# Kernel tuning notes

Hardware: AMD Instinct MI355X
Metric: run time of the kernel (lower is better)

## Reference

```python
import jax, jax.numpy as jnp
import numpy as np

HIDDEN = 128
N_RBF = 32
LMAX = 2
N_NODES = 10000
DEG = 8  # each node has DEG outgoing (and DEG incoming) edges on a ring


def _build_graph():
    src = np.repeat(np.arange(N_NODES, dtype=np.int64), DEG)
    offs = np.tile(np.arange(1, DEG + 1, dtype=np.int64), N_NODES)
    dst = (src + offs) % N_NODES
    keys = src * N_NODES + dst
    order = np.argsort(keys)
    src2, dst2 = src[order], dst[order]  # e2 sorted by key (searchsorted invariant)
    e1_to_e2 = np.empty_like(order)
    e1_to_e2[order] = np.arange(order.size)
    return src, dst, src2, dst2, e1_to_e2


def setup_inputs() -> dict:
    key = jax.random.key(0)
    ks = jax.random.split(key, 12)
    src1, dst1, src2, dst2, e1_to_e2 = _build_graph()
    E1, E2 = src1.size, src2.size
    in_dim = 6 * HIDDEN + 3 * N_RBF + 1  # 865

    def lin(k, fi, fo):
        kw, kb = jax.random.split(k)
        s = 1.0 / np.sqrt(fi)
        return (jax.random.uniform(kw, (fi, fo), minval=-s, maxval=s),
                jax.random.uniform(kb, (fo,), minval=-s, maxval=s))

    w1, b1 = lin(ks[0], in_dim, HIDDEN)
    w2, b2 = lin(ks[1], HIDDEN, HIDDEN)
    wgw, bgw = lin(ks[2], HIDDEN, HIDDEN)
    wgt, bgt = lin(ks[3], HIDDEN, HIDDEN)
    return {
        "t_e2": jax.random.normal(ks[4], (E2, HIDDEN), dtype=jnp.float32),
        "h": jax.random.normal(ks[5], (N_NODES, HIDDEN), dtype=jnp.float32),
        "edge_index1": jnp.asarray(np.stack([src1, dst1])),
        "edge_index2": jnp.asarray(np.stack([src2, dst2])),
        "e1_to_e2": jnp.asarray(e1_to_e2),
        "dist_e1": jax.random.uniform(ks[6], (E1,), dtype=jnp.float32),
        "dist_e2": jax.random.uniform(ks[7], (E2,), dtype=jnp.float32),
        "rbf_e1": jax.random.normal(ks[8], (E1, N_RBF), dtype=jnp.float32),
        "rbf_e2": jax.random.normal(ks[9], (E2, N_RBF), dtype=jnp.float32),
        "sph_e1": jax.random.normal(ks[10], (E1, LMAX + 1), dtype=jnp.float32),
        "num_nodes": N_NODES,
        "w1": w1, "b1": b1, "w2": w2, "b2": b2,
        "wgw": wgw, "bgw": bgw, "wgt": wgt, "bgt": bgt,
    }


def _wedge_indices(edge_index1, edge_index2, num_nodes):
    """Host-side (numpy, vectorized) wedge construction: for every center node k,
    all (incoming edge i->k, outgoing edge k->j) pairs with i != j, kept only when
    (i, j) itself is an edge in e2 (looked up by sorted key search)."""
    src1 = np.asarray(edge_index1[0]); dst1 = np.asarray(edge_index1[1])
    src2 = np.asarray(edge_index2[0]); dst2 = np.asarray(edge_index2[1])
    nz = src1 != dst1  # drop self-loops
    s, d = src1[nz], dst1[nz]
    eid = np.nonzero(nz)[0]
    out_deg = np.bincount(s, minlength=num_nodes)
    out_order = np.argsort(s, kind="stable")  # filtered-edge positions grouped by src
    out_ptr = np.concatenate([np.zeros(1, np.int64), np.cumsum(out_deg)])
    reps = out_deg[d]  # each incoming edge pairs with out_deg[center] outgoing edges
    total = int(reps.sum())
    if total == 0:
        z = np.zeros(0, np.int64)
        return z, z, z, z, z, z
    starts = np.cumsum(reps) - reps
    local = np.arange(total) - np.repeat(starts, reps)
    kj_f = out_order[np.repeat(out_ptr[d], reps) + local]
    i = np.repeat(s, reps)
    k = np.repeat(d, reps)
    eik = np.repeat(eid, reps)
    j = d[kj_f]
    ekj = eid[kj_f]
    m = i != j
    i, k, j, eik, ekj = i[m], k[m], j[m], eik[m], ekj[m]
    e2_keys = src2.astype(np.int64) * num_nodes + dst2
    pk = i.astype(np.int64) * num_nodes + j
    pos = np.searchsorted(e2_keys, pk)
    posc = np.minimum(pos, e2_keys.size - 1)
    valid = (pos < e2_keys.size) & (e2_keys[posc] == pk)
    return i[valid], k[valid], j[valid], eik[valid], ekj[valid], posc[valid]


def reference(t_e2, h, edge_index1, edge_index2, e1_to_e2, dist_e1, dist_e2,
              rbf_e1, rbf_e2, sph_e1, num_nodes,
              w1, b1, w2, b2, wgw, bgw, wgt, bgt):
    i, k, j, eik, ekj, eij = _wedge_indices(edge_index1, edge_index2, int(num_nodes))
    if i.size == 0:
        return t_e2
    i, k, j = jnp.asarray(i), jnp.asarray(k), jnp.asarray(j)
    eik, ekj, eij = jnp.asarray(eik), jnp.asarray(ekj), jnp.asarray(eij)
    e1e2 = jnp.asarray(e1_to_e2)
    # wedge geometric features (wedge_use_high_degree=False -> l=1 contraction only)
    c_feat = (sph_e1[eik, 1] * sph_e1[ekj, 1])[:, None]           # [W, 1]
    g = jnp.concatenate([rbf_e1[eik], rbf_e1[ekj], rbf_e2[eij], c_feat], axis=-1)
    rho_in = jnp.concatenate([t_e2[e1e2[eik]], t_e2[e1e2[ekj]], t_e2[eij],
                              h[i], h[k], h[j], g], axis=-1)       # [W, 865]
    msg = jax.nn.silu(rho_in @ w1 + b1) @ w2 + b2                  # [W, H]
    m = jax.ops.segment_sum(msg, eij, num_segments=t_e2.shape[0])  # [E2, H]
    return t_e2 + jax.nn.sigmoid(m @ wgw + bgw) * jnp.tanh(t_e2 @ wgt + bgt)
```

## Files before the change

### kernel.cpp

```cpp
#include <hip/hip_runtime.h>
#include <math.h>

typedef unsigned short u16;
typedef unsigned int u32;
typedef __bf16 bf16x8 __attribute__((ext_vector_type(8)));
typedef float f32x4 __attribute__((ext_vector_type(4)));

__device__ __forceinline__ float bf2f(u16 v){ union{u32 u;float f;}c; c.u=((u32)v)<<16; return c.f; }
__device__ __forceinline__ u16 f2bf(float f){ union{float f;u32 u;}c; c.f=f; u32 l=(c.u>>16)&1u; c.u+=0x7fffu+l; return (u16)(c.u>>16); }
__device__ __forceinline__ u32 pk2(float a, float b){ return (u32)f2bf(a) | ((u32)f2bf(b)<<16); }
__device__ __forceinline__ uint4 ld8f(const float* p){
  float4 x = ((const float4*)p)[0];
  float4 y = ((const float4*)p)[1];
  uint4 r; r.x=pk2(x.x,x.y); r.y=pk2(x.z,x.w); r.z=pk2(y.x,y.y); r.w=pk2(y.z,y.w);
  return r;
}
__device__ __forceinline__ float fsilu(float x){ return x/(1.f+__expf(-x)); }


__global__ void k_setup_edges(const int* __restrict__ e1_to_e2,
                              const float* __restrict__ rbf_e1,
                              const float* __restrict__ sph_e1,
                              u16* __restrict__ rbf1p,
                              float* __restrict__ sph_c, int E1) {
  int e = blockIdx.x*256 + threadIdx.x;
  if (e >= E1) return;
  int f = e1_to_e2[e];
  sph_c[f] = sph_e1[e*3+1];
  const float* s = rbf_e1 + (size_t)e*32;
  uint4* d = (uint4*)(rbf1p + (size_t)f*32);
  d[0]=ld8f(s); d[1]=ld8f(s+8); d[2]=ld8f(s+16); d[3]=ld8f(s+24);
}

__global__ void k_out_ptr(const int* __restrict__ src2, int* __restrict__ out_ptr,
                          int Nn, int E2) {
  int n = blockIdx.x*256 + threadIdx.x;
  if (n > Nn) return;
  int lo=0, hi=E2;
  while (lo<hi){ int m=(lo+hi)>>1; if (src2[m]<n) lo=m+1; else hi=m; }
  out_ptr[n]=lo;
}

__global__ void k_wbigt(const float* __restrict__ w1, u16* __restrict__ WbigT) {
  int id = blockIdx.x*256+threadIdx.x;
  if (id >= 384*448) return;
  int n = id/448, k = id%448;
  int q = n>>7, nn = n&127;
  int row = -1;
  if (k<128) row = q*128+k;
  else if (k<256) { if (q==0) row = 384+(k-128); }
  else if (k<384) { if (q==0) row = 512+(k-256); else if (q==1) row = 640+(k-256); }
  else if (k<416) { if (q==0) row = 768+(k-384); else if (q==1) row = 800+(k-384); }
  else { if (q==2) row = 832+(k-416); }
  WbigT[id] = (row>=0) ? f2bf(w1[row*128+nn]) : (u16)0;
}

__global__ void k_smallw(const float* __restrict__ w2, const float* __restrict__ wgw,
                         const float* __restrict__ wgt, const float* __restrict__ b2,
                         u16* __restrict__ WcT, u16* __restrict__ WgtT,
                         float* __restrict__ bc2) {
  int id = blockIdx.x*256+threadIdx.x;
  if (id < 16384) {
    int n = id&127, k = id>>7;
    float s = 0.f;
    for (int r=0;r<128;r++) s += w2[k*128+r]*wgw[r*128+n];
    WcT[n*128+k] = f2bf(s);
    WgtT[n*128+k] = f2bf(wgt[k*128+n]);
  } else if (id < 16384+128) {
    int n = id-16384;
    float s = 0.f;
    for (int r=0;r<128;r++) s += b2[r]*wgw[r*128+n];
    bc2[n] = s;
  }
}

__global__ __launch_bounds__(256, 8)
void k_enum(const int* __restrict__ src2, const int* __restrict__ dst2,
            const int* __restrict__ out_ptr, const float* __restrict__ sph_c,
            int4* __restrict__ wrec, int* __restrict__ cnt, int E2) {
  int id = blockIdx.x*256 + threadIdx.x;
  if (id >= E2*8) return;
  int gw = id >> 3, d = id & 7;
  int i = src2[gw], j = dst2[gw];
  int f = out_ptr[i] + d;
  if (f >= out_ptr[i+1]) return;
  int k = dst2[f];
  int lo = out_ptr[k], hi = out_ptr[k+1], hi0 = hi;
  while (lo<hi) { int m=(lo+hi)>>1; if (dst2[m]<j) lo=m+1; else hi=m; }
  if (lo < hi0 && dst2[lo]==j) {
    float cf = sph_c[f]*sph_c[lo];
    int slot = atomicAdd(&cnt[gw], 1);
    int4 r; r.x=f; r.y=lo; r.z=__float_as_int(cf); r.w=0;
    wrec[(size_t)gw*8 + slot] = r;
  }
}

__global__ __launch_bounds__(256, 8)
void k_wedge2(const u16* __restrict__ Q1, const u16* __restrict__ Q2,
              const u16* __restrict__ P3, const int4* __restrict__ wrec,
              const int* __restrict__ cnt, const float* __restrict__ w1,
              u16* __restrict__ S, int E2) {
  int gw = (int)((blockIdx.x*256 + threadIdx.x) >> 6);
  int lane = threadIdx.x & 63;
  if (gw >= E2) return;
  u32 p3u = ((const u32*)(P3 + (size_t)gw*128))[lane];
  float p30 = bf2f((u16)(p3u&0xffff)), p31 = bf2f((u16)(p3u>>16));
  float2 wv = ((const float2*)(w1 + 864*128))[lane];
  const u32* q1b = (const u32*)Q1;
  const u32* q2b = (const u32*)Q2;
  const int4* wr = wrec + (size_t)gw*8;
  int c = cnt[gw];
  float a0=0.f, a1=0.f;
  int w = 0;
  for (; w+2<=c; w+=2) {
    int4 rA = wr[w], rB = wr[w+1];
    u32 xA = q1b[(size_t)rA.x*64 + lane];
    u32 yA = q2b[(size_t)rA.y*64 + lane];
    u32 xB = q1b[(size_t)rB.x*64 + lane];
    u32 yB = q2b[(size_t)rB.y*64 + lane];
    float cfA = __int_as_float(rA.z), cfB = __int_as_float(rB.z);
    float x0 = p30 + bf2f((u16)(xA&0xffff)) + bf2f((u16)(yA&0xffff)) + cfA*wv.x;
    float x1 = p31 + bf2f((u16)(xA>>16))    + bf2f((u16)(yA>>16))    + cfA*wv.y;
    float z0 = p30 + bf2f((u16)(xB&0xffff)) + bf2f((u16)(yB&0xffff)) + cfB*wv.x;
    float z1 = p31 + bf2f((u16)(xB>>16))    + bf2f((u16)(yB>>16))    + cfB*wv.y;
    a0 += fsilu(x0) + fsilu(z0);
    a1 += fsilu(x1) + fsilu(z1);
  }
  if (w < c) {
    int4 rA = wr[w];
    u32 xA = q1b[(size_t)rA.x*64 + lane];
    u32 yA = q2b[(size_t)rA.y*64 + lane];
    float cfA = __int_as_float(rA.z);
    float x0 = p30 + bf2f((u16)(xA&0xffff)) + bf2f((u16)(yA&0xffff)) + cfA*wv.x;
    float x1 = p31 + bf2f((u16)(xA>>16))    + bf2f((u16)(yA>>16))    + cfA*wv.y;
    a0 += fsilu(x0);
    a1 += fsilu(x1);
  }
  ((u32*)(S + (size_t)gw*128))[lane] = pk2(a0, a1);
}

struct GArgs {
  const float* t_f32; const float* h; const float* rbf_e2;
  const u16* rbf1p; const u16* Asrc;
  const int* src2; const int* dst2; const int* cnt;
  const u16* Bmat; const u16* Gin;
  const float* b1; const float* bgw; const float* bgt; const float* bc2;
  u16* out0; u16* out1; u16* out2;
  float* outf;
  int M;
};

template<int MODE>
__global__ __launch_bounds__(256, 2)
void k_gemm(GArgs a) {
  constexpr int KT = (MODE==0)?448:128;
  constexpr int NK = KT/32;
  __shared__ u16 As[128*40];
  __shared__ u16 Bs[128*40];
  const int tid = threadIdx.x;
  const int bm = blockIdx.x, bn = blockIdx.y;
  const int lane = tid & 63, wave = tid >> 6;
  const int wm = wave >> 1, wn = wave & 1;
  const int quad = lane >> 4, l16 = lane & 15;

  const int part = tid & 3;
  const int ra = tid >> 2;
  const int rb = ra + 64;
  long fa = (long)bm*128 + ra;
  long fb = (long)bm*128 + rb;
  if (fa >= a.M) fa = a.M-1;
  if (fb >= a.M) fb = a.M-1;
  int sa=0, da=0, sb=0, db=0;
  if constexpr (MODE==0) { sa=a.src2[fa]; da=a.dst2[fa]; sb=a.src2[fb]; db=a.dst2[fb]; }

  f32x4 acc[4][4] = {};
  for (int ks=0; ks<NK; ks++) {
    const int kb = ks*32;
    uint4 va, vb;
    if constexpr (MODE==0) {
      if (ks<4)       { va = ld8f(a.t_f32 + fa*128 + kb + part*8);
                        vb = ld8f(a.t_f32 + fb*128 + kb + part*8); }
      else if (ks<8)  { va = ld8f(a.h + (long)sa*128 + (kb-128) + part*8);
                        vb = ld8f(a.h + (long)sb*128 + (kb-128) + part*8); }
      else if (ks<12) { va = ld8f(a.h + (long)da*128 + (kb-256) + part*8);
                        vb = ld8f(a.h + (long)db*128 + (kb-256) + part*8); }
      else if (ks==12){ va = *(const uint4*)(a.rbf1p + fa*32 + part*8);
                        vb = *(const uint4*)(a.rbf1p + fb*32 + part*8); }
      else            { va = ld8f(a.rbf_e2 + fa*32 + part*8);
                        vb = ld8f(a.rbf_e2 + fb*32 + part*8); }
    } else if constexpr (MODE==1) {
      va = *(const uint4*)(a.Asrc + fa*128 + kb + part*8);
      vb = *(const uint4*)(a.Asrc + fb*128 + kb + part*8);
    } else {
      va = ld8f(a.t_f32 + fa*128 + kb + part*8);
      vb = ld8f(a.t_f32 + fb*128 + kb + part*8);
    }
    uint4 wa = *(const uint4*)(a.Bmat + (long)(bn*128 + ra)*KT + kb + part*8);
    uint4 wb = *(const uint4*)(a.Bmat + (long)(bn*128 + rb)*KT + kb + part*8);
    __syncthreads();
    *(uint4*)(As + ra*40 + part*8) = va;
    *(uint4*)(As + rb*40 + part*8) = vb;
    *(uint4*)(Bs + ra*40 + part*8) = wa;
    *(uint4*)(Bs + rb*40 + part*8) = wb;
    __syncthreads();
    bf16x8 af[4], bfr[4];
    #pragma unroll
    for (int t=0;t<4;t++) {
      af[t]  = *(const bf16x8*)(As + (wm*64 + t*16 + l16)*40 + quad*8);
      bfr[t] = *(const bf16x8*)(Bs + (wn*64 + t*16 + l16)*40 + quad*8);
    }
    #pragma unroll
    for (int tm=0;tm<4;tm++)
      #pragma unroll
      for (int tn=0;tn<4;tn++)
        acc[tm][tn] = __builtin_amdgcn_mfma_f32_16x16x32_bf16(af[tm], bfr[tn], acc[tm][tn], 0,0,0);
  }

  #pragma unroll
  for (int tm=0;tm<4;tm++) {
    const int rloc = wm*64 + tm*16 + quad*4;
    #pragma unroll
    for (int r=0;r<4;r++) {
      long row = (long)bm*128 + rloc + r;
      if (row >= a.M) continue;
      #pragma unroll
      for (int tn=0;tn<4;tn++) {
        const int col = wn*64 + tn*16 + l16;
        float v = acc[tm][tn][r];
        if constexpr (MODE==0) {
          u16* dst = (bn==0)? a.out0 : (bn==1)? a.out1 : a.out2;
          if (bn==2) v += a.b1[col];
          dst[row*128 + col] = f2bf(v);
        } else if constexpr (MODE==1) {
          float u = v + (float)a.cnt[row]*a.bc2[col] + a.bgw[col];
          float g = 1.f/(1.f+__expf(-u));
          a.out0[row*128+col] = f2bf(g);
        } else {
          float vv = v + a.bgt[col];
          float th = 1.f - 2.f/(__expf(2.f*vv)+1.f);
          float t  = a.t_f32[row*128+col];
          float g  = bf2f(a.Gin[row*128+col]);
          a.outf[row*128+col] = t + g*th;
        }
      }
    }
  }
}

extern "C" void kernel_launch(void* const* d_in, const int* in_sizes, int n_in,
                              void* d_out, int out_size, void* d_ws, size_t ws_size,
                              hipStream_t stream) {
  const float* t_e2  = (const float*)d_in[0];
  const float* h     = (const float*)d_in[1];
  const int* ei2     = (const int*)d_in[3];
  const int* e1_to_e2 = (const int*)d_in[4];
  const float* rbf_e1 = (const float*)d_in[7];
  const float* rbf_e2 = (const float*)d_in[8];
  const float* sph_e1 = (const float*)d_in[9];
  const float* w1  = (const float*)d_in[11];
  const float* b1  = (const float*)d_in[12];
  const float* w2  = (const float*)d_in[13];
  const float* b2  = (const float*)d_in[14];
  const float* wgw = (const float*)d_in[15];
  const float* bgw = (const float*)d_in[16];
  const float* wgt = (const float*)d_in[17];
  const float* bgt = (const float*)d_in[18];

  const int E2 = in_sizes[0]/128;
  const int Nn = in_sizes[1]/128;
  const int E1 = in_sizes[5];
  const int* src2 = ei2;
  const int* dst2 = ei2 + E2;

  char* p = (char*)d_ws;
  u16* Q1 = (u16*)p;       p += (size_t)E2*128*2;
  u16* Q2 = (u16*)p;       p += (size_t)E2*128*2;
  u16* P3 = (u16*)p;       p += (size_t)E2*128*2;
  u16* rbf1p = (u16*)p;    p += (size_t)E2*32*2;
  u16* WbigT = (u16*)p;    p += (size_t)384*448*2;
  u16* WcT   = (u16*)p;    p += (size_t)128*128*2;
  u16* WgtT  = (u16*)p;    p += (size_t)128*128*2;
  float* sph_c = (float*)p; p += (size_t)E2*4;
  float* bc2   = (float*)p; p += 512;
  int* out_ptr = (int*)p;   p += (((size_t)(Nn+1)*4 + 63)/64)*64;
  int* cnt     = (int*)p;   p += (size_t)E2*4;
  int4* wrec   = (int4*)p;  p += (size_t)E2*8*16;
  u16* S = P3;
  u16* G = Q1;

  hipMemsetAsync(cnt, 0, (size_t)E2*4, stream);

  k_setup_edges<<<(E1+255)/256, 256, 0, stream>>>(e1_to_e2, rbf_e1, sph_e1, rbf1p, sph_c, E1);
  k_out_ptr<<<(Nn+1+255)/256, 256, 0, stream>>>(src2, out_ptr, Nn, E2);
  k_wbigt<<<(384*448+255)/256, 256, 0, stream>>>(w1, WbigT);
  k_smallw<<<(16512+255)/256, 256, 0, stream>>>(w2, wgw, wgt, b2, WcT, WgtT, bc2);
  k_enum<<<(E2*8+255)/256, 256, 0, stream>>>(src2, dst2, out_ptr, sph_c, wrec, cnt, E2);

  const int Mb = (E2+127)/128;
  {
    GArgs a = {};
    a.t_f32=t_e2; a.h=h; a.rbf1p=rbf1p; a.rbf_e2=rbf_e2;
    a.src2=src2; a.dst2=dst2; a.Bmat=WbigT; a.b1=b1;
    a.out0=Q1; a.out1=Q2; a.out2=P3; a.M=E2;
    k_gemm<0><<<dim3(Mb,3), 256, 0, stream>>>(a);
  }
  k_wedge2<<<(E2+3)/4, 256, 0, stream>>>(Q1, Q2, P3, wrec, cnt, w1, S, E2);
  {
    GArgs a = {};
    a.Asrc=S; a.cnt=cnt; a.Bmat=WcT; a.bgw=bgw; a.bc2=bc2;
    a.out0=G; a.M=E2;
    k_gemm<1><<<dim3(Mb,1), 256, 0, stream>>>(a);
  }
  {
    GArgs a = {};
    a.t_f32=t_e2; a.Bmat=WgtT; a.bgt=bgt; a.Gin=G;
    a.outf=(float*)d_out; a.M=E2;
    k_gemm<2><<<dim3(Mb,1), 256, 0, stream>>>(a);
  }
}
```

Baseline: 330.1 us.

## Pre-convert fp32 inputs to bf16 and double-buffer GEMM shared-memory tiles

```diff
diff --git a/kernel.cpp b/kernel.cpp
--- a/kernel.cpp
+++ b/kernel.cpp
@@ -17,6 +17,21 @@
 }
 __device__ __forceinline__ float fsilu(float x){ return x/(1.f+__expf(-x)); }
 
+
+__global__ __launch_bounds__(256, 8)
+void k_cvt(const float* __restrict__ t, const float* __restrict__ h,
+           const float* __restrict__ r2, u16* __restrict__ T16,
+           u16* __restrict__ h16, u16* __restrict__ rbf2b,
+           long n_t, long n_h, long n_r) {
+  long base = ((long)blockIdx.x*256 + threadIdx.x)*8;
+  if (base < n_t) {
+    *(uint4*)(T16+base) = ld8f(t+base);
+  } else if (base < n_t+n_h) {
+    long o = base-n_t;  *(uint4*)(h16+o) = ld8f(h+o);
+  } else if (base < n_t+n_h+n_r) {
+    long o = base-n_t-n_h; *(uint4*)(rbf2b+o) = ld8f(r2+o);
+  }
+}
 
 __global__ void k_setup_edges(const int* __restrict__ e1_to_e2,
                               const float* __restrict__ rbf_e1,
@@ -140,8 +155,9 @@
 }
 
 struct GArgs {
-  const float* t_f32; const float* h; const float* rbf_e2;
-  const u16* rbf1p; const u16* Asrc;
+  const float* t_f32;
+  const u16* T16; const u16* h16; const u16* rbf1p; const u16* rbf2b;
+  const u16* Asrc;
   const int* src2; const int* dst2; const int* cnt;
   const u16* Bmat; const u16* Gin;
   const float* b1; const float* bgw; const float* bgt; const float* bc2;
@@ -155,8 +171,8 @@
 void k_gemm(GArgs a) {
   constexpr int KT = (MODE==0)?448:128;
   constexpr int NK = KT/32;
-  __shared__ u16 As[128*40];
-  __shared__ u16 Bs[128*40];
+  __shared__ u16 As[2][128*40];
+  __shared__ u16 Bs[2][128*40];
   const int tid = threadIdx.x;
   const int bm = blockIdx.x, bn = blockIdx.y;
   const int lane = tid & 63, wave = tid >> 6;
@@ -173,47 +189,67 @@
   int sa=0, da=0, sb=0, db=0;
   if constexpr (MODE==0) { sa=a.src2[fa]; da=a.dst2[fa]; sb=a.src2[fb]; db=a.dst2[fb]; }
 
+  auto aptr = [&](int ks, long f, int sn, int dn) -> const u16* {
+    const int kb = ks*32;
+    if constexpr (MODE==0) {
+      if (ks<4)   return a.T16 + f*128 + kb + part*8;
+      if (ks<8)   return a.h16 + (long)sn*128 + (kb-128) + part*8;
+      if (ks<12)  return a.h16 + (long)dn*128 + (kb-256) + part*8;
+      if (ks==12) return a.rbf1p + f*32 + part*8;
+      return a.rbf2b + f*32 + part*8;
+    } else if constexpr (MODE==1) {
+      return a.Asrc + f*128 + kb + part*8;
+    } else {
+      return a.T16 + f*128 + kb + part*8;
+    }
+  };
+  const u16* Bbase_a = a.Bmat + (long)(bn*128 + ra)*KT + part*8;
+  const u16* Bbase_b = a.Bmat + (long)(bn*128 + rb)*KT + part*8;
+
+  uint4 ga = *(const uint4*)aptr(0, fa, sa, da);
+  uint4 gb = *(const uint4*)aptr(0, fb, sb, db);
+  uint4 wa = *(const uint4*)(Bbase_a);
+  uint4 wb = *(const uint4*)(Bbase_b);
+  *(uint4*)(As[0] + ra*40 + part*8) = ga;
+  *(uint4*)(As[0] + rb*40 + part*8) = gb;
+  *(uint4*)(Bs[0] + ra*40 + part*8) = wa;
+  *(uint4*)(Bs[0] + rb*40 + part*8) = wb;
+  if (NK > 1) {
+    ga = *(const uint4*)aptr(1, fa, sa, da);
+    gb = *(const uint4*)aptr(1, fb, sb, db);
+    wa = *(const uint4*)(Bbase_a + 32);
+    wb = *(const uint4*)(Bbase_b + 32);
+  }
+  __syncthreads();
+
   f32x4 acc[4][4] = {};
+  #pragma unroll
   for (int ks=0; ks<NK; ks++) {
-    const int kb = ks*32;
-    uint4 va, vb;
-    if constexpr (MODE==0) {
-      if (ks<4)       { va = ld8f(a.t_f32 + fa*128 + kb + part*8);
-                        vb = ld8f(a.t_f32 + fb*128 + kb + part*8); }
-      else if (ks<8)  { va = ld8f(a.h + (long)sa*128 + (kb-128) + part*8);
-                        vb = ld8f(a.h + (long)sb*128 + (kb-128) + part*8); }
-      else if (ks<12) { va = ld8f(a.h + (long)da*128 + (kb-256) + part*8);
-                        vb = ld8f(a.h + (long)db*128 + (kb-256) + part*8); }
-      else if (ks==12){ va = *(const uint4*)(a.rbf1p + fa*32 + part*8);
-                        vb = *(const uint4*)(a.rbf1p + fb*32 + part*8); }
-      else            { va = ld8f(a.rbf_e2 + fa*32 + part*8);
-                        vb = ld8f(a.rbf_e2 + fb*32 + part*8); }
-    } else if constexpr (MODE==1) {
-      va = *(const uint4*)(a.Asrc + fa*128 + kb + part*8);
-      vb = *(const uint4*)(a.Asrc + fb*128 + kb + part*8);
-    } else {
-      va = ld8f(a.t_f32 + fa*128 + kb + part*8);
-      vb = ld8f(a.t_f32 + fb*128 + kb + part*8);
-    }
-    uint4 wa = *(const uint4*)(a.Bmat + (long)(bn*128 + ra)*KT + kb + part*8);
-    uint4 wb = *(const uint4*)(a.Bmat + (long)(bn*128 + rb)*KT + kb + part*8);
-    __syncthreads();
-    *(uint4*)(As + ra*40 + part*8) = va;
-    *(uint4*)(As + rb*40 + part*8) = vb;
-    *(uint4*)(Bs + ra*40 + part*8) = wa;
-    *(uint4*)(Bs + rb*40 + part*8) = wb;
-    __syncthreads();
+    const int buf = ks & 1, nxt = buf ^ 1;
+    if (ks+1 < NK) {
+      *(uint4*)(As[nxt] + ra*40 + part*8) = ga;
+      *(uint4*)(As[nxt] + rb*40 + part*8) = gb;
+      *(uint4*)(Bs[nxt] + ra*40 + part*8) = wa;
+      *(uint4*)(Bs[nxt] + rb*40 + part*8) = wb;
+    }
+    if (ks+2 < NK) {
+      ga = *(const uint4*)aptr(ks+2, fa, sa, da);
+      gb = *(const uint4*)aptr(ks+2, fb, sb, db);
+      wa = *(const uint4*)(Bbase_a + (ks+2)*32);
+      wb = *(const uint4*)(Bbase_b + (ks+2)*32);
+    }
     bf16x8 af[4], bfr[4];
     #pragma unroll
     for (int t=0;t<4;t++) {
-      af[t]  = *(const bf16x8*)(As + (wm*64 + t*16 + l16)*40 + quad*8);
-      bfr[t] = *(const bf16x8*)(Bs + (wn*64 + t*16 + l16)*40 + quad*8);
+      af[t]  = *(const bf16x8*)(As[buf] + (wm*64 + t*16 + l16)*40 + quad*8);
+      bfr[t] = *(const bf16x8*)(Bs[buf] + (wn*64 + t*16 + l16)*40 + quad*8);
     }
     #pragma unroll
     for (int tm=0;tm<4;tm++)
       #pragma unroll
       for (int tn=0;tn<4;tn++)
         acc[tm][tn] = __builtin_amdgcn_mfma_f32_16x16x32_bf16(af[tm], bfr[tn], acc[tm][tn], 0,0,0);
+    __syncthreads();
   }
 
   #pragma unroll
@@ -276,6 +312,9 @@
   u16* Q1 = (u16*)p;       p += (size_t)E2*128*2;
   u16* Q2 = (u16*)p;       p += (size_t)E2*128*2;
   u16* P3 = (u16*)p;       p += (size_t)E2*128*2;
+  u16* T16 = (u16*)p;      p += (size_t)E2*128*2;
+  u16* h16 = (u16*)p;      p += (size_t)Nn*128*2;
+  u16* rbf2b = (u16*)p;    p += (size_t)E2*32*2;
   u16* rbf1p = (u16*)p;    p += (size_t)E2*32*2;
   u16* WbigT = (u16*)p;    p += (size_t)384*448*2;
   u16* WcT   = (u16*)p;    p += (size_t)128*128*2;
@@ -290,6 +329,9 @@
 
   hipMemsetAsync(cnt, 0, (size_t)E2*4, stream);
 
+  long n_t = (long)E2*128, n_h = (long)Nn*128, n_r = (long)E2*32;
+  long tot8 = (n_t+n_h+n_r)/8;
+  k_cvt<<<(int)((tot8+255)/256), 256, 0, stream>>>(t_e2, h, rbf_e2, T16, h16, rbf2b, n_t, n_h, n_r);
   k_setup_edges<<<(E1+255)/256, 256, 0, stream>>>(e1_to_e2, rbf_e1, sph_e1, rbf1p, sph_c, E1);
   k_out_ptr<<<(Nn+1+255)/256, 256, 0, stream>>>(src2, out_ptr, Nn, E2);
   k_wbigt<<<(384*448+255)/256, 256, 0, stream>>>(w1, WbigT);
@@ -299,7 +341,7 @@
   const int Mb = (E2+127)/128;
   {
     GArgs a = {};
-    a.t_f32=t_e2; a.h=h; a.rbf1p=rbf1p; a.rbf_e2=rbf_e2;
+    a.T16=T16; a.h16=h16; a.rbf1p=rbf1p; a.rbf2b=rbf2b;
     a.src2=src2; a.dst2=dst2; a.Bmat=WbigT; a.b1=b1;
     a.out0=Q1; a.out1=Q2; a.out2=P3; a.M=E2;
     k_gemm<0><<<dim3(Mb,3), 256, 0, stream>>>(a);
@@ -313,7 +355,7 @@
   }
   {
     GArgs a = {};
-    a.t_f32=t_e2; a.Bmat=WgtT; a.bgt=bgt; a.Gin=G;
+    a.T16=T16; a.t_f32=t_e2; a.Bmat=WgtT; a.bgt=bgt; a.Gin=G;
     a.outf=(float*)d_out; a.M=E2;
     k_gemm<2><<<dim3(Mb,1), 256, 0, stream>>>(a);
   }
```

Result: no change. 333.9 us (+1.2%).
